# Kernel optimization log

Measured on AMD Instinct MI355X. Metric: run time of the kernel, lower is better.

Reference implementation:

```python
import jax, jax.numpy as jnp
import numpy as np

N_NODES = 2_000_000
N_MOVABLE = 1_800_000
PINS_PER_NODE = 4
N_PINS = N_NODES * PINS_PER_NODE  # 8M
N_NETS = 2_000_000


def setup_inputs() -> dict:
    rng = np.random.default_rng(0)
    # node -> pin CSR: constant degree for simplicity, pins are a permutation
    flat_node2pin_start = np.arange(0, N_PINS + 1, PINS_PER_NODE, dtype=np.int32)
    flat_node2pin = rng.permutation(N_PINS).astype(np.int32)
    # each pin belongs to one net
    pin2net_map = rng.integers(0, N_NETS, size=N_PINS, dtype=np.int64)
    # net -> pin CSR starts, consistent with pin2net_map (only degrees are used)
    counts = np.bincount(pin2net_map, minlength=N_NETS)
    flat_net2pin = np.concatenate([[0], np.cumsum(counts)]).astype(np.int32)
    net_weights = rng.uniform(0.5, 2.0, size=N_NETS).astype(np.float32)  # exercise clamp(min=1.0)
    return {
        "net_weights": jnp.asarray(net_weights),
        "flat_node2pin_start": jnp.asarray(flat_node2pin_start),
        "flat_node2pin": jnp.asarray(flat_node2pin),
        "pin2net_map": jnp.asarray(pin2net_map.astype(np.int32)),
        "flat_net2pin": jnp.asarray(flat_net2pin),
        "num_movable_nodes": N_MOVABLE,
    }


def reference(net_weights, flat_node2pin_start, flat_node2pin, pin2net_map, flat_net2pin, num_movable_nodes):
    num_nodes = flat_node2pin_start.shape[0] - 1
    num_pins = flat_node2pin.shape[0]
    w = jnp.maximum(net_weights, 1.0)  # torch.clamp(net_weights, min=1.0)
    # segment id (owning node) for each slot in flat_node2pin, from CSR starts
    seg = jnp.searchsorted(flat_node2pin_start[1:], jnp.arange(num_pins), side="right")
    net = pin2net_map[flat_node2pin]              # pin -> net (double indirection)
    deg = flat_net2pin[net + 1] - flat_net2pin[net]  # net degree
    contrib = jnp.where(deg > 1, w[net] / jnp.maximum(deg - 1, 1).astype(w.dtype), 0.0)
    contrib = jnp.where(seg < num_movable_nodes, contrib, 0.0)  # only movable nodes
    out = jax.ops.segment_sum(contrib, seg, num_segments=num_nodes)
    return out
```

## Files before the change

kernel.cpp:

```cpp
#include <hip/hip_runtime.h>
#include <hip/hip_fp16.h>


typedef int          vint4  __attribute__((ext_vector_type(4)));
typedef unsigned int vuint2 __attribute__((ext_vector_type(2)));

#define NT_LOAD(x)      __builtin_nontemporal_load(&(x))
#define NT_STORE(x, v)  __builtin_nontemporal_store((v), &(x))

static constexpr float kScale   = 2.0f / 255.0f;
static constexpr float kInvStep = 127.5f;

__global__ __launch_bounds__(256) void net_value_u8_kernel(
    const float* __restrict__ net_weights,
    const int*   __restrict__ net2pin_start,
    unsigned char* __restrict__ v_u8,
    int num_nets)
{
    int n = blockIdx.x * blockDim.x + threadIdx.x;
    if (n >= num_nets) return;
    int a = NT_LOAD(net2pin_start[n]);
    int b = NT_LOAD(net2pin_start[n + 1]);
    int d = b - a;
    int code = 0;
    if (d > 1) {
        float w = fmaxf(NT_LOAD(net_weights[n]), 1.0f);
        float val = w / (float)(d - 1);
        code = (int)(val * kInvStep + 0.5f);
        code = min(code, 255);
    }
    NT_STORE(v_u8[n], (unsigned char)code);
}

__global__ __launch_bounds__(256) void pin_value_kernel(
    const int*           __restrict__ pin2net,
    const unsigned char* __restrict__ v_u8,
    unsigned char*       __restrict__ pin_value,
    int num_pins)
{
    int t = blockIdx.x * blockDim.x + threadIdx.x;
    int p0 = t * 8;
    if (p0 + 7 < num_pins) {
        vint4 n0 = NT_LOAD(((const vint4*)pin2net)[2 * t]);
        vint4 n1 = NT_LOAD(((const vint4*)pin2net)[2 * t + 1]);
        vuint2 packed;
        packed.x =  (unsigned int)v_u8[(unsigned int)n0.x]
                 | ((unsigned int)v_u8[(unsigned int)n0.y] << 8)
                 | ((unsigned int)v_u8[(unsigned int)n0.z] << 16)
                 | ((unsigned int)v_u8[(unsigned int)n0.w] << 24);
        packed.y =  (unsigned int)v_u8[(unsigned int)n1.x]
                 | ((unsigned int)v_u8[(unsigned int)n1.y] << 8)
                 | ((unsigned int)v_u8[(unsigned int)n1.z] << 16)
                 | ((unsigned int)v_u8[(unsigned int)n1.w] << 24);
        NT_STORE(((vuint2*)pin_value)[t], packed);
    } else if (p0 < num_pins) {
        for (int p = p0; p < num_pins; ++p)
            NT_STORE(pin_value[p], v_u8[(unsigned int)NT_LOAD(pin2net[p])]);
    }
}

__global__ __launch_bounds__(256) void sweep_lower_kernel(
    const int*           __restrict__ node2pin_start,
    const int*           __restrict__ node2pin,
    const unsigned char* __restrict__ pin_value,
    const int*           __restrict__ num_movable_ptr,
    unsigned short*      __restrict__ partial,
    int num_nodes, int H)
{
    int i = blockIdx.x * blockDim.x + threadIdx.x;
    if (i >= num_nodes) return;
    const int num_movable = num_movable_ptr[0];
    int c = 0;
    if (i < num_movable) {
        int s = node2pin_start[i];
        int e = node2pin_start[i + 1];
        if (e - s == 4 && (s & 3) == 0) {
            vint4 pins = NT_LOAD(((const vint4*)node2pin)[s >> 2]);
            if (pins.x < H) c += (int)pin_value[(unsigned int)pins.x];
            if (pins.y < H) c += (int)pin_value[(unsigned int)pins.y];
            if (pins.z < H) c += (int)pin_value[(unsigned int)pins.z];
            if (pins.w < H) c += (int)pin_value[(unsigned int)pins.w];
        } else {
            for (int p = s; p < e; ++p) {
                int pin = NT_LOAD(node2pin[p]);
                if (pin < H) c += (int)pin_value[(unsigned int)pin];
            }
        }
    }
    NT_STORE(partial[i], (unsigned short)c);
}

__global__ __launch_bounds__(256) void sweep_upper_kernel(
    const int*            __restrict__ node2pin_start,
    const int*            __restrict__ node2pin,
    const unsigned char*  __restrict__ pin_value,
    const int*            __restrict__ num_movable_ptr,
    const unsigned short* __restrict__ partial,
    float*                __restrict__ out,
    int num_nodes, int H)
{
    int i = blockIdx.x * blockDim.x + threadIdx.x;
    if (i >= num_nodes) return;
    const int num_movable = num_movable_ptr[0];
    int c = (int)NT_LOAD(partial[i]);
    if (i < num_movable) {
        int s = node2pin_start[i];
        int e = node2pin_start[i + 1];
        if (e - s == 4 && (s & 3) == 0) {
            vint4 pins = NT_LOAD(((const vint4*)node2pin)[s >> 2]);
            if (pins.x >= H) c += (int)pin_value[(unsigned int)pins.x];
            if (pins.y >= H) c += (int)pin_value[(unsigned int)pins.y];
            if (pins.z >= H) c += (int)pin_value[(unsigned int)pins.z];
            if (pins.w >= H) c += (int)pin_value[(unsigned int)pins.w];
        } else {
            for (int p = s; p < e; ++p) {
                int pin = NT_LOAD(node2pin[p]);
                if (pin >= H) c += (int)pin_value[(unsigned int)pin];
            }
        }
    }
    NT_STORE(out[i], kScale * (float)c);
}

__global__ __launch_bounds__(256) void precond_wl_sum_kernel(
    const int*           __restrict__ node2pin_start,
    const int*           __restrict__ node2pin,
    const unsigned char* __restrict__ pin_value,
    const int*           __restrict__ num_movable_ptr,
    float*               __restrict__ out,
    int num_nodes)
{
    int i = blockIdx.x * blockDim.x + threadIdx.x;
    if (i >= num_nodes) return;
    const int num_movable = num_movable_ptr[0];
    float acc = 0.0f;
    if (i < num_movable) {
        int s = node2pin_start[i];
        int e = node2pin_start[i + 1];
        int c = 0;
        if (e - s == 4 && (s & 3) == 0) {
            vint4 pins = NT_LOAD(((const vint4*)node2pin)[s >> 2]);
            c = (int)pin_value[(unsigned int)pins.x] + (int)pin_value[(unsigned int)pins.y]
              + (int)pin_value[(unsigned int)pins.z] + (int)pin_value[(unsigned int)pins.w];
        } else {
            for (int p = s; p < e; ++p)
                c += (int)pin_value[(unsigned int)NT_LOAD(node2pin[p])];
        }
        acc = kScale * (float)c;
    }
    NT_STORE(out[i], acc);
}

__global__ __launch_bounds__(256) void net_value_f16_kernel(
    const float* __restrict__ net_weights,
    const int*   __restrict__ net2pin_start,
    __half*      __restrict__ v,
    int num_nets)
{
    int n = blockIdx.x * blockDim.x + threadIdx.x;
    if (n >= num_nets) return;
    int a = net2pin_start[n];
    int b = net2pin_start[n + 1];
    int d = b - a;
    float val = 0.0f;
    if (d > 1) {
        float w = fmaxf(net_weights[n], 1.0f);
        val = w / (float)(d - 1);
    }
    v[n] = __float2half(val);
}

__global__ __launch_bounds__(256) void precond_wl_gather_f16_kernel(
    const int*    __restrict__ node2pin_start,
    const int*    __restrict__ node2pin,
    const int*    __restrict__ pin2net,
    const __half* __restrict__ v,
    const int*    __restrict__ num_movable_ptr,
    float*        __restrict__ out,
    int num_nodes)
{
    int i = blockIdx.x * blockDim.x + threadIdx.x;
    if (i >= num_nodes) return;
    const int num_movable = num_movable_ptr[0];
    float acc = 0.0f;
    if (i < num_movable) {
        int s = node2pin_start[i];
        int e = node2pin_start[i + 1];
        for (int p = s; p < e; ++p)
            acc += __half2float(v[(unsigned int)pin2net[(unsigned int)node2pin[p]]]);
    }
    out[i] = acc;
}

extern "C" void kernel_launch(void* const* d_in, const int* in_sizes, int n_in,
                              void* d_out, int out_size, void* d_ws, size_t ws_size,
                              hipStream_t stream)
{
    const float* net_weights     = (const float*)d_in[0];
    const int*   node2pin_start  = (const int*)d_in[1];
    const int*   node2pin        = (const int*)d_in[2];
    const int*   pin2net         = (const int*)d_in[3];
    const int*   net2pin_start   = (const int*)d_in[4];
    const int*   num_movable_ptr = (const int*)d_in[5];

    const int num_nodes = in_sizes[1] - 1;
    const int num_pins  = in_sizes[2];
    const int num_nets  = in_sizes[4] - 1;

    const int block = 256;
    const int grid_nodes = (num_nodes + block - 1) / block;
    const int grid_nets  = (num_nets + block - 1) / block;
    const int grid_pin8  = ((num_pins + 7) / 8 + block - 1) / block;

    size_t pv_off  = ((size_t)num_nets + 255) & ~(size_t)255;
    size_t pt_off  = (pv_off + (size_t)num_pins + 255) & ~(size_t)255;
    size_t need3   = pv_off + (size_t)num_pins;
    size_t need4   = pt_off + (size_t)num_nodes * sizeof(unsigned short);

    if (ws_size >= need3) {
        unsigned char* v_u8      = (unsigned char*)d_ws;
        unsigned char* pin_value = (unsigned char*)d_ws + pv_off;

        net_value_u8_kernel<<<grid_nets, block, 0, stream>>>(
            net_weights, net2pin_start, v_u8, num_nets);
        pin_value_kernel<<<grid_pin8, block, 0, stream>>>(
            pin2net, v_u8, pin_value, num_pins);

        if (ws_size >= need4) {
            unsigned short* partial = (unsigned short*)((unsigned char*)d_ws + pt_off);
            const int H = num_pins >> 1;
            sweep_lower_kernel<<<grid_nodes, block, 0, stream>>>(
                node2pin_start, node2pin, pin_value, num_movable_ptr,
                partial, num_nodes, H);
            sweep_upper_kernel<<<grid_nodes, block, 0, stream>>>(
                node2pin_start, node2pin, pin_value, num_movable_ptr,
                partial, (float*)d_out, num_nodes, H);
        } else {
            precond_wl_sum_kernel<<<grid_nodes, block, 0, stream>>>(
                node2pin_start, node2pin, pin_value, num_movable_ptr,
                (float*)d_out, num_nodes);
        }
    } else {
        __half* v = (__half*)d_ws;
        net_value_f16_kernel<<<grid_nets, block, 0, stream>>>(
            net_weights, net2pin_start, v, num_nets);
        precond_wl_gather_f16_kernel<<<grid_nodes, block, 0, stream>>>(
            node2pin_start, node2pin, pin2net, v, num_movable_ptr,
            (float*)d_out, num_nodes);
    }
}
```

Before: 204.3 us.

## Fuse all stages into one cooperative persistent kernel with grid syncs

Replaces the four separate launches (net value, pin value, lower and upper half sweeps) with one cooperative kernel of 1024x256 threads that uses grid.sync between phases. Each thread keeps up to eight nodes' pin indices and partial sums in registers across the lower/upper sweep, so the 16-bit partial buffer round-trip and the extra launches go away. In exchange it relies on cooperative-launch residency and pays for three grid-wide barriers. It also gives up the massive thread-level parallelism the latency-bound gathers had before. The old kernels remain as a fallback, and the small-workspace fallback path now passes a reinterpreted buffer as the partial input.

```diff
diff --git a/kernel.cpp b/kernel.cpp
--- a/kernel.cpp
+++ b/kernel.cpp
@@ -1,5 +1,8 @@
 #include <hip/hip_runtime.h>
 #include <hip/hip_fp16.h>
+#include <hip/hip_cooperative_groups.h>
+
+namespace cg = cooperative_groups;
 
 
 typedef int          vint4  __attribute__((ext_vector_type(4)));
@@ -10,6 +13,111 @@
 
 static constexpr float kScale   = 2.0f / 255.0f;
 static constexpr float kInvStep = 127.5f;
+
+#define COOP_BLOCKS  1024
+#define COOP_THREADS 256
+#define MAX_ITERS    8
+
+__global__ __launch_bounds__(COOP_THREADS, 4) void precond_coop_kernel(
+    const float* __restrict__ net_weights,
+    const int*   __restrict__ net2pin_start,
+    const int*   __restrict__ node2pin_start,
+    const int*   __restrict__ node2pin,
+    const int*   __restrict__ pin2net,
+    const int*   __restrict__ num_movable_ptr,
+    unsigned char* __restrict__ v_u8,
+    unsigned char* __restrict__ pin_value,
+    float*       __restrict__ out,
+    int num_nets, int num_pins, int num_nodes)
+{
+    cg::grid_group grid = cg::this_grid();
+    const int T = COOP_BLOCKS * COOP_THREADS;
+    const int t = blockIdx.x * COOP_THREADS + threadIdx.x;
+
+    for (int n = t; n < num_nets; n += T) {
+        int a = NT_LOAD(net2pin_start[n]);
+        int b = NT_LOAD(net2pin_start[n + 1]);
+        int d = b - a;
+        int code = 0;
+        if (d > 1) {
+            float w = fmaxf(NT_LOAD(net_weights[n]), 1.0f);
+            code = (int)(w / (float)(d - 1) * kInvStep + 0.5f);
+            code = min(code, 255);
+        }
+        NT_STORE(v_u8[n], (unsigned char)code);
+    }
+    grid.sync();
+
+    {
+        const int ngrp = num_pins >> 3;
+        for (int g = t; g < ngrp; g += T) {
+            vint4 n0 = NT_LOAD(((const vint4*)pin2net)[2 * g]);
+            vint4 n1 = NT_LOAD(((const vint4*)pin2net)[2 * g + 1]);
+            vuint2 packed;
+            packed.x =  (unsigned int)v_u8[(unsigned int)n0.x]
+                     | ((unsigned int)v_u8[(unsigned int)n0.y] << 8)
+                     | ((unsigned int)v_u8[(unsigned int)n0.z] << 16)
+                     | ((unsigned int)v_u8[(unsigned int)n0.w] << 24);
+            packed.y =  (unsigned int)v_u8[(unsigned int)n1.x]
+                     | ((unsigned int)v_u8[(unsigned int)n1.y] << 8)
+                     | ((unsigned int)v_u8[(unsigned int)n1.z] << 16)
+                     | ((unsigned int)v_u8[(unsigned int)n1.w] << 24);
+            NT_STORE(((vuint2*)pin_value)[g], packed);
+        }
+        for (int p = (ngrp << 3) + t; p < num_pins; p += T)
+            NT_STORE(pin_value[p], v_u8[(unsigned int)NT_LOAD(pin2net[p])]);
+    }
+    grid.sync();
+
+    const int num_movable = num_movable_ptr[0];
+    const int H = num_pins >> 1;
+    const int iters = min((num_nodes - 1) / T + 1, MAX_ITERS);
+
+    vint4 pins[MAX_ITERS];
+    int   c[MAX_ITERS];
+
+    for (int it = 0; it < iters; ++it) {
+        int i = it * T + t;
+        c[it] = 0;
+        pins[it].x = -1; pins[it].y = -1; pins[it].z = -1; pins[it].w = -1;
+        if (i < num_movable) {
+            int s = node2pin_start[i];
+            int e = node2pin_start[i + 1];
+            if (e - s == 4 && (s & 3) == 0) {
+                pins[it] = NT_LOAD(((const vint4*)node2pin)[s >> 2]);
+            } else {
+                int cc = 0;
+                for (int p = s; p < e; ++p)
+                    cc += (int)pin_value[(unsigned int)NT_LOAD(node2pin[p])];
+                c[it] = cc;
+            }
+        }
+    }
+
+    for (int it = 0; it < iters; ++it) {
+        vint4 p = pins[it];
+        int cc = c[it];
+        if (p.x >= 0 && p.x < H) cc += (int)pin_value[(unsigned int)p.x];
+        if (p.y >= 0 && p.y < H) cc += (int)pin_value[(unsigned int)p.y];
+        if (p.z >= 0 && p.z < H) cc += (int)pin_value[(unsigned int)p.z];
+        if (p.w >= 0 && p.w < H) cc += (int)pin_value[(unsigned int)p.w];
+        c[it] = cc;
+    }
+
+    grid.sync();
+
+    for (int it = 0; it < iters; ++it) {
+        vint4 p = pins[it];
+        int cc = c[it];
+        if (p.x >= H) cc += (int)pin_value[(unsigned int)p.x];
+        if (p.y >= H) cc += (int)pin_value[(unsigned int)p.y];
+        if (p.z >= H) cc += (int)pin_value[(unsigned int)p.z];
+        if (p.w >= H) cc += (int)pin_value[(unsigned int)p.w];
+        int i = it * T + t;
+        if (i < num_nodes) NT_STORE(out[i], kScale * (float)cc);
+    }
+}
+
 
 __global__ __launch_bounds__(256) void net_value_u8_kernel(
     const float* __restrict__ net_weights,
@@ -25,8 +133,7 @@
     int code = 0;
     if (d > 1) {
         float w = fmaxf(NT_LOAD(net_weights[n]), 1.0f);
-        float val = w / (float)(d - 1);
-        code = (int)(val * kInvStep + 0.5f);
+        code = (int)(w / (float)(d - 1) * kInvStep + 0.5f);
         code = min(code, 255);
     }
     NT_STORE(v_u8[n], (unsigned char)code);
@@ -122,35 +229,6 @@
     NT_STORE(out[i], kScale * (float)c);
 }
 
-__global__ __launch_bounds__(256) void precond_wl_sum_kernel(
-    const int*           __restrict__ node2pin_start,
-    const int*           __restrict__ node2pin,
-    const unsigned char* __restrict__ pin_value,
-    const int*           __restrict__ num_movable_ptr,
-    float*               __restrict__ out,
-    int num_nodes)
-{
-    int i = blockIdx.x * blockDim.x + threadIdx.x;
-    if (i >= num_nodes) return;
-    const int num_movable = num_movable_ptr[0];
-    float acc = 0.0f;
-    if (i < num_movable) {
-        int s = node2pin_start[i];
-        int e = node2pin_start[i + 1];
-        int c = 0;
-        if (e - s == 4 && (s & 3) == 0) {
-            vint4 pins = NT_LOAD(((const vint4*)node2pin)[s >> 2]);
-            c = (int)pin_value[(unsigned int)pins.x] + (int)pin_value[(unsigned int)pins.y]
-              + (int)pin_value[(unsigned int)pins.z] + (int)pin_value[(unsigned int)pins.w];
-        } else {
-            for (int p = s; p < e; ++p)
-                c += (int)pin_value[(unsigned int)NT_LOAD(node2pin[p])];
-        }
-        acc = kScale * (float)c;
-    }
-    NT_STORE(out[i], acc);
-}
-
 __global__ __launch_bounds__(256) void net_value_f16_kernel(
     const float* __restrict__ net_weights,
     const int*   __restrict__ net2pin_start,
@@ -214,31 +292,50 @@
 
     size_t pv_off  = ((size_t)num_nets + 255) & ~(size_t)255;
     size_t pt_off  = (pv_off + (size_t)num_pins + 255) & ~(size_t)255;
-    size_t need3   = pv_off + (size_t)num_pins;
+    size_t need2   = pv_off + (size_t)num_pins;
     size_t need4   = pt_off + (size_t)num_nodes * sizeof(unsigned short);
 
-    if (ws_size >= need3) {
+    if (ws_size >= need2) {
         unsigned char* v_u8      = (unsigned char*)d_ws;
         unsigned char* pin_value = (unsigned char*)d_ws + pv_off;
-
-        net_value_u8_kernel<<<grid_nets, block, 0, stream>>>(
-            net_weights, net2pin_start, v_u8, num_nets);
-        pin_value_kernel<<<grid_pin8, block, 0, stream>>>(
-            pin2net, v_u8, pin_value, num_pins);
-
-        if (ws_size >= need4) {
-            unsigned short* partial = (unsigned short*)((unsigned char*)d_ws + pt_off);
-            const int H = num_pins >> 1;
-            sweep_lower_kernel<<<grid_nodes, block, 0, stream>>>(
-                node2pin_start, node2pin, pin_value, num_movable_ptr,
-                partial, num_nodes, H);
-            sweep_upper_kernel<<<grid_nodes, block, 0, stream>>>(
-                node2pin_start, node2pin, pin_value, num_movable_ptr,
-                partial, (float*)d_out, num_nodes, H);
-        } else {
-            precond_wl_sum_kernel<<<grid_nodes, block, 0, stream>>>(
-                node2pin_start, node2pin, pin_value, num_movable_ptr,
-                (float*)d_out, num_nodes);
+        float*         out_f     = (float*)d_out;
+
+        bool coop_ok = false;
+        const int T = COOP_BLOCKS * COOP_THREADS;
+        if ((num_nodes - 1) / T + 1 <= MAX_ITERS) {
+            int nn = num_nets, np = num_pins, nd = num_nodes;
+            void* args[] = {
+                (void*)&net_weights, (void*)&net2pin_start,
+                (void*)&node2pin_start, (void*)&node2pin, (void*)&pin2net,
+                (void*)&num_movable_ptr, (void*)&v_u8, (void*)&pin_value,
+                (void*)&out_f, (void*)&nn, (void*)&np, (void*)&nd };
+            hipError_t err = hipLaunchCooperativeKernel(
+                (const void*)precond_coop_kernel,
+                dim3(COOP_BLOCKS), dim3(COOP_THREADS), args, 0, stream);
+            coop_ok = (err == hipSuccess);
+        }
+
+        if (!coop_ok) {
+            net_value_u8_kernel<<<grid_nets, block, 0, stream>>>(
+                net_weights, net2pin_start, v_u8, num_nets);
+            pin_value_kernel<<<grid_pin8, block, 0, stream>>>(
+                pin2net, v_u8, pin_value, num_pins);
+            if (ws_size >= need4) {
+                unsigned short* partial =
+                    (unsigned short*)((unsigned char*)d_ws + pt_off);
+                const int H = num_pins >> 1;
+                sweep_lower_kernel<<<grid_nodes, block, 0, stream>>>(
+                    node2pin_start, node2pin, pin_value, num_movable_ptr,
+                    partial, num_nodes, H);
+                sweep_upper_kernel<<<grid_nodes, block, 0, stream>>>(
+                    node2pin_start, node2pin, pin_value, num_movable_ptr,
+                    partial, out_f, num_nodes, H);
+            } else {
+                sweep_upper_kernel<<<grid_nodes, block, 0, stream>>>(
+                    node2pin_start, node2pin, pin_value, num_movable_ptr,
+                    (const unsigned short*)v_u8 , out_f,
+                    num_nodes, 0);
+            }
         }
     } else {
         __half* v = (__half*)d_ws;
```

After: 562.7 us. 2.75x slower.
